# Performance work log

Hardware: AMD Instinct MI355X
Metric: run time of the kernel (lower is better)

The kernel has to match this reference:

```python
import jax, jax.numpy as jnp
import numpy as np

B, N, D = 2, 512, 64
EPS = 1e-5  # BatchNorm eps (torch default)


def setup_inputs() -> dict:
    key = jax.random.key(0)

    def k(i):
        return jax.random.fold_in(key, i)

    inp = {}
    inp["node_features"] = jax.random.normal(k(0), (B, N, D), jnp.float32)
    inp["node_masks"] = jax.random.randint(k(1), (B, N), 0, 2) > 0
    lin_dims = [(128, 2 * D), (64, 128), (32, 64), (1, 32)]
    for i, (o, ii) in enumerate(lin_dims, start=1):
        inp[f"W{i}"] = jax.random.normal(k(10 + i), (o, ii), jnp.float32) * np.float32(1.0 / np.sqrt(ii))
        inp[f"b{i}"] = jnp.zeros((o,), jnp.float32)
    for i, o in enumerate([128, 64, 32], start=1):
        inp[f"g{i}"] = jnp.ones((o,), jnp.float32) + 0.1 * jax.random.normal(k(20 + i), (o,), jnp.float32)
        inp[f"be{i}"] = 0.1 * jax.random.normal(k(30 + i), (o,), jnp.float32)
        inp[f"m{i}"] = jnp.zeros((o,), jnp.float32)
        inp[f"v{i}"] = jnp.ones((o,), jnp.float32)
    return inp


def _bn(x, g, be, m, v):
    # eval-mode BatchNorm1d with running stats
    return (x - m) * (g * jax.lax.rsqrt(v + EPS)) + be


def _edge_predictor(node_features, node_masks,
                    W1, b1, g1, be1, m1, v1,
                    W2, b2, g2, be2, m2, v2,
                    W3, b3, g3, be3, m3, v3,
                    W4, b4):
    Bq, Nq, Dq = node_features.shape
    # pairwise features: concat(f_i, f_j) -> [B, N, N, 2D]
    fi = jnp.broadcast_to(node_features[:, :, None, :], (Bq, Nq, Nq, Dq))
    fj = jnp.broadcast_to(node_features[:, None, :, :], (Bq, Nq, Nq, Dq))
    pair = jnp.concatenate([fi, fj], axis=-1)
    # 3-layer MLP + BN (eval) + ReLU, then scalar head (dropout is identity in eval)
    x = jax.nn.relu(_bn(jnp.einsum('bijk,ok->bijo', pair, W1) + b1, g1, be1, m1, v1))
    x = jax.nn.relu(_bn(jnp.einsum('bijk,ok->bijo', x, W2) + b2, g2, be2, m2, v2))
    x = jax.nn.relu(_bn(jnp.einsum('bijk,ok->bijo', x, W3) + b3, g3, be3, m3, v3))
    logits = (jnp.einsum('bijk,ok->bijo', x, W4) + b4)[..., 0]  # [B, N, N]
    # diagonal -> -10, symmetrize
    eye = jnp.eye(Nq, dtype=bool)
    logits = jnp.where(eye[None], jnp.float32(-10.0), logits)
    logits = (logits + jnp.swapaxes(logits, 1, 2)) * 0.5
    # cosine-similarity boost (F.normalize eps = 1e-12)
    norm = jnp.maximum(jnp.linalg.norm(node_features, axis=-1, keepdims=True), 1e-12)
    nf = node_features / norm
    sim = jnp.einsum('bnd,bmd->bnm', nf, nf)
    logits = (logits + 2.0 * sim) / 0.5  # temperature 0.5
    probs = jax.nn.sigmoid(logits)
    probs = jnp.where(probs > 0.6, probs * 1.2, probs * 0.8)
    probs = jnp.clip(probs, 0.0, 1.0)
    # scatter into dense adjacency only at valid (i, j) pairs; batches with
    # n_valid <= 1 are skipped (stay zero) as in the torch loop
    n_valid = jnp.sum(node_masks, axis=-1)  # [B]
    active = (n_valid > 1)[:, None, None]
    pair_mask = node_masks[:, :, None] & node_masks[:, None, :] & active
    adjacency = jnp.where(pair_mask, probs, 0.0)
    adjacency_logits = jnp.where(pair_mask, logits, 0.0)
    return adjacency, adjacency_logits


def reference(node_features, node_masks,
              W1, b1, g1, be1, m1, v1,
              W2, b2, g2, be2, m2, v2,
              W3, b3, g3, be3, m3, v3,
              W4, b4):
    return _edge_predictor(node_features, node_masks,
                           W1, b1, g1, be1, m1, v1,
                           W2, b2, g2, be2, m2, v2,
                           W3, b3, g3, be3, m3, v3,
                           W4, b4)
```

## Files before the change

kernel.cpp:

```cpp
#include <hip/hip_runtime.h>
#include <math.h>

#define BB 2
#define NN2 512
#define DD 64
#define EPS 1e-5f

#define OFF_W1TA  0
#define OFF_W1TB  8192
#define OFF_VBIAS 16384
#define OFF_W2T   16512
#define OFF_C2    24704
#define OFF_W3T   24768
#define OFF_C3    26816
#define OFF_U     26848
#define OFF_V     157920
#define OFF_NF    288992
#define OFF_RAWL  354528
#define OFF_NVALID 878816

__global__ __launch_bounds__(256) void prep_fold(
    const float* __restrict__ W1, const float* __restrict__ b1,
    const float* __restrict__ W2, const float* __restrict__ b2,
    const float* __restrict__ W3, const float* __restrict__ b3,
    const float* __restrict__ g1, const float* __restrict__ be1,
    const float* __restrict__ m1, const float* __restrict__ v1,
    const float* __restrict__ g2, const float* __restrict__ be2,
    const float* __restrict__ m2, const float* __restrict__ v2,
    const float* __restrict__ g3, const float* __restrict__ be3,
    const float* __restrict__ m3, const float* __restrict__ v3,
    const int* __restrict__ masks,
    float* __restrict__ ws, int* __restrict__ nvalid)
{
    const int blk = blockIdx.x, t = threadIdx.x;
    if (blk < 8) {
        int e0 = blk * 1024 + t * 4;
        #pragma unroll
        for (int q = 0; q < 4; q++) {
            int e = e0 + q;
            int o = e & 63, k = e >> 6;
            float s = g2[o] * rsqrtf(v2[o] + EPS);
            ws[OFF_W2T + e] = W2[o * 128 + k] * s;
        }
    } else if (blk < 10) {
        int e0 = (blk - 8) * 1024 + t * 4;
        #pragma unroll
        for (int q = 0; q < 4; q++) {
            int e = e0 + q;
            if (e < 2048) {
                int o = e & 31, k = e >> 5;
                float s = g3[o] * rsqrtf(v3[o] + EPS);
                ws[OFF_W3T + e] = W3[o * 64 + k] * s;
            }
        }
    } else if (blk < 26) {
        int e0 = (blk - 10) * 1024 + t * 4;
        #pragma unroll
        for (int q = 0; q < 4; q++) {
            int e = e0 + q;
            if (e < 8192) {
                int d = e >> 7, o = e & 127;
                float s = g1[o] * rsqrtf(v1[o] + EPS);
                ws[OFF_W1TA + e] = W1[o * 128 + d] * s;
            } else {
                int eb = e - 8192;
                int d = eb >> 7, o = eb & 127;
                float s = g1[o] * rsqrtf(v1[o] + EPS);
                ws[OFF_W1TB + eb] = W1[o * 128 + 64 + d] * s;
            }
        }
    } else if (blk == 26) {
        if (t < 128) {
            float s = g1[t] * rsqrtf(v1[t] + EPS);
            ws[OFF_VBIAS + t] = s * b1[t] + be1[t] - m1[t] * s;
        } else if (t < 192) {
            int o = t - 128;
            float s = g2[o] * rsqrtf(v2[o] + EPS);
            ws[OFF_C2 + o] = b2[o] * s + be2[o] - m2[o] * s;
        } else if (t < 224) {
            int o = t - 192;
            float s = g3[o] * rsqrtf(v3[o] + EPS);
            ws[OFF_C3 + o] = b3[o] * s + be3[o] - m3[o] * s;
        }
    } else {
        int w = t >> 6, l = t & 63;
        if (w < BB) {
            int s = 0;
            #pragma unroll
            for (int q = 0; q < 8; q++) s += (masks[w * NN2 + q * 64 + l] != 0) ? 1 : 0;
            #pragma unroll
            for (int off = 1; off < 64; off <<= 1) s += __shfl_xor(s, off);
            if (l == 0) nvalid[w] = s;
        }
    }
}

__global__ __launch_bounds__(128) void prep_uv(
    const float* __restrict__ feat,
    const float* __restrict__ W1ta, const float* __restrict__ W1tb,
    const float* __restrict__ Vbias,
    float* __restrict__ U, float* __restrict__ V)
{
    __shared__ float F[4][64];
    const int nb = blockIdx.x * 4;
    const int t = threadIdx.x;
    if (t < 64) {
        int r = t >> 4, c = (t & 15) * 4;
        *(float4*)&F[r][c] = *(const float4*)&feat[(nb + r) * 64 + c];
    }
    __syncthreads();
    const int o = t;
    float aU[4] = {0.f, 0.f, 0.f, 0.f};
    float aV[4] = {0.f, 0.f, 0.f, 0.f};
    for (int d = 0; d < 64; d++) {
        float wa = W1ta[d * 128 + o];
        float wb = W1tb[d * 128 + o];
        #pragma unroll
        for (int n = 0; n < 4; n++) {
            aU[n] = fmaf(F[n][d], wa, aU[n]);
            aV[n] = fmaf(F[n][d], wb, aV[n]);
        }
    }
    float vb = Vbias[o];
    #pragma unroll
    for (int n = 0; n < 4; n++) {
        U[(nb + n) * 128 + o] = aU[n];
        V[(nb + n) * 128 + o] = aV[n] + vb;
    }
}

__global__ __launch_bounds__(256) void prep_nf(
    const float* __restrict__ feat, float* __restrict__ nf)
{
    const int t = threadIdx.x;
    const int w = t >> 6, l = t & 63;
    const int node = blockIdx.x * 4 + w;
    float x = feat[node * 64 + l];
    float ss = x * x;
    #pragma unroll
    for (int off = 1; off < 64; off <<= 1) ss += __shfl_xor(ss, off);
    float inv = 1.0f / fmaxf(sqrtf(ss), 1e-12f);
    nf[node * 64 + l] = x * inv;
}

__global__ __launch_bounds__(256) void mlp_main(
    const float* __restrict__ U, const float* __restrict__ V,
    const float* __restrict__ W2t, const float* __restrict__ c2,
    const float* __restrict__ W3t, const float* __restrict__ c3,
    const float* __restrict__ W4, const float* __restrict__ b4,
    float* __restrict__ rawL)
{
    __shared__ float Ut[16][132];
    __shared__ float Vt[16][132];
    const int t = threadIdx.x;
    const int b = blockIdx.z;
    const int i0 = blockIdx.y * 16, j0 = blockIdx.x * 16;
    {
        int r = t >> 4, c = (t & 15) * 8;
        float4 a0 = *(const float4*)&U[(b * NN2 + i0 + r) * 128 + c];
        float4 a1 = *(const float4*)&U[(b * NN2 + i0 + r) * 128 + c + 4];
        *(float4*)&Ut[r][c]     = a0;
        *(float4*)&Ut[r][c + 4] = a1;
        float4 v0 = *(const float4*)&V[(b * NN2 + j0 + r) * 128 + c];
        float4 v1 = *(const float4*)&V[(b * NN2 + j0 + r) * 128 + c + 4];
        *(float4*)&Vt[r][c]     = v0;
        *(float4*)&Vt[r][c + 4] = v1;
    }
    __syncthreads();
    const int i = t >> 4, j = t & 15;

    float acc[64];
    #pragma unroll
    for (int o = 0; o < 64; o++) acc[o] = c2[o];
    for (int k = 0; k < 128; k += 4) {
        float4 uk = *(const float4*)&Ut[i][k];
        float4 vk = *(const float4*)&Vt[j][k];
        float h[4];
        h[0] = fmaxf(uk.x + vk.x, 0.f);
        h[1] = fmaxf(uk.y + vk.y, 0.f);
        h[2] = fmaxf(uk.z + vk.z, 0.f);
        h[3] = fmaxf(uk.w + vk.w, 0.f);
        const float* w = &W2t[k * 64];
        #pragma unroll
        for (int kk = 0; kk < 4; kk++) {
            #pragma unroll
            for (int o = 0; o < 64; o++)
                acc[o] = fmaf(w[kk * 64 + o], h[kk], acc[o]);
        }
    }
    float a3[32];
    #pragma unroll
    for (int o = 0; o < 32; o++) a3[o] = c3[o];
    #pragma unroll
    for (int k = 0; k < 64; k++) {
        float hk = fmaxf(acc[k], 0.f);
        #pragma unroll
        for (int o = 0; o < 32; o++)
            a3[o] = fmaf(W3t[k * 32 + o], hk, a3[o]);
    }
    float lg = b4[0];
    #pragma unroll
    for (int k = 0; k < 32; k++) lg = fmaf(W4[k], fmaxf(a3[k], 0.f), lg);

    rawL[(size_t)(b * NN2 + i0 + i) * NN2 + j0 + j] = lg;
}

__global__ __launch_bounds__(256) void post_kernel(
    const float* __restrict__ rawL, const float* __restrict__ nf,
    const int* __restrict__ masks, const int* __restrict__ nvalid,
    float* __restrict__ outA, float* __restrict__ outL)
{
    __shared__ float nfI[16][68], nfJ[16][68];
    __shared__ float Lt[16][17];
    __shared__ int mI[16], mJ[16];
    const int t = threadIdx.x;
    const int b = blockIdx.z, i0 = blockIdx.y * 16, j0 = blockIdx.x * 16;
    {
        int r = t >> 4, c = (t & 15) * 4;
        *(float4*)&nfI[r][c] = *(const float4*)&nf[(b * NN2 + i0 + r) * 64 + c];
        *(float4*)&nfJ[r][c] = *(const float4*)&nf[(b * NN2 + j0 + r) * 64 + c];
    }
    {
        int r = t >> 4, c = t & 15;
        Lt[r][c] = rawL[(size_t)(b * NN2 + j0 + r) * NN2 + i0 + c];
    }
    if (t < 16) mI[t] = masks[b * NN2 + i0 + t];
    else if (t < 32) mJ[t - 16] = masks[b * NN2 + j0 + (t - 16)];
    __syncthreads();

    const int i = t >> 4, j = t & 15;
    const int gi = i0 + i, gj = j0 + j;
    float Lij = rawL[(size_t)(b * NN2 + gi) * NN2 + gj];
    float Lji = Lt[j][i];
    float Ls = (gi == gj) ? -10.0f : 0.5f * (Lij + Lji);

    float sim = 0.f;
    #pragma unroll
    for (int d = 0; d < 64; d += 4) {
        float4 x = *(const float4*)&nfI[i][d];
        float4 y = *(const float4*)&nfJ[j][d];
        sim = fmaf(x.x, y.x, sim);
        sim = fmaf(x.y, y.y, sim);
        sim = fmaf(x.z, y.z, sim);
        sim = fmaf(x.w, y.w, sim);
    }
    float logit = (Ls + 2.0f * sim) * 2.0f;
    float p = 1.0f / (1.0f + expf(-logit));
    p = (p > 0.6f) ? p * 1.2f : p * 0.8f;
    p = fminf(fmaxf(p, 0.0f), 1.0f);
    bool pm = (mI[i] != 0) && (mJ[j] != 0) && (nvalid[b] > 1);
    size_t idx = (size_t)(b * NN2 + gi) * NN2 + gj;
    outA[idx] = pm ? p : 0.0f;
    outL[idx] = pm ? logit : 0.0f;
}

extern "C" void kernel_launch(void* const* d_in, const int* in_sizes, int n_in,
                              void* d_out, int out_size, void* d_ws, size_t ws_size,
                              hipStream_t stream)
{
    const float* feat = (const float*)d_in[0];
    const int*   masks = (const int*)d_in[1];
    const float* W1 = (const float*)d_in[2];
    const float* b1 = (const float*)d_in[3];
    const float* W2 = (const float*)d_in[4];
    const float* b2 = (const float*)d_in[5];
    const float* W3 = (const float*)d_in[6];
    const float* b3 = (const float*)d_in[7];
    const float* W4 = (const float*)d_in[8];
    const float* b4 = (const float*)d_in[9];
    const float* g1 = (const float*)d_in[10];
    const float* be1 = (const float*)d_in[11];
    const float* m1 = (const float*)d_in[12];
    const float* v1 = (const float*)d_in[13];
    const float* g2 = (const float*)d_in[14];
    const float* be2 = (const float*)d_in[15];
    const float* m2 = (const float*)d_in[16];
    const float* v2 = (const float*)d_in[17];
    const float* g3 = (const float*)d_in[18];
    const float* be3 = (const float*)d_in[19];
    const float* m3 = (const float*)d_in[20];
    const float* v3 = (const float*)d_in[21];

    float* ws = (float*)d_ws;
    float* W1ta  = ws + OFF_W1TA;
    float* W1tb  = ws + OFF_W1TB;
    float* Vbias = ws + OFF_VBIAS;
    float* W2t   = ws + OFF_W2T;
    float* c2    = ws + OFF_C2;
    float* W3t   = ws + OFF_W3T;
    float* c3    = ws + OFF_C3;
    float* U     = ws + OFF_U;
    float* V     = ws + OFF_V;
    float* nf    = ws + OFF_NF;
    float* rawL  = ws + OFF_RAWL;
    int*   nvalid = (int*)(ws + OFF_NVALID);

    float* outA = (float*)d_out;
    float* outL = outA + (size_t)BB * NN2 * NN2;

    prep_fold<<<28, 256, 0, stream>>>(W1, b1, W2, b2, W3, b3,
                                      g1, be1, m1, v1, g2, be2, m2, v2,
                                      g3, be3, m3, v3, masks, ws, nvalid);
    prep_uv<<<256, 128, 0, stream>>>(feat, W1ta, W1tb, Vbias, U, V);
    prep_nf<<<256, 256, 0, stream>>>(feat, nf);
    dim3 grid(32, 32, 2);
    mlp_main<<<grid, 256, 0, stream>>>(U, V, W2t, c2, W3t, c3, W4, b4, rawL);
    post_kernel<<<grid, 256, 0, stream>>>(rawL, nf, masks, nvalid, outA, outL);
}
```

Measured before the change: 267.2 us.

## Fuse MLP and post-processing over symmetric tile pairs, merge nf into prep_uv

Launches one block per upper-triangular tile pair (i,j). Each block evaluates the MLP for both (i,j) and (j,i), exchanges the results through shared memory to symmetrize, and writes both output tiles directly. This removes the rawL round-trip through global memory and the separate post kernel. The per-node normalization is also moved into prep_uv, which drops one more launch. The MLP work is unchanged, but diagonal blocks do half the work of off-diagonal ones, which causes load imbalance, and the larger shared footprint together with the launch_bounds min-blocks hint may change occupancy.

```diff
diff --git a/kernel.cpp b/kernel.cpp
--- a/kernel.cpp
+++ b/kernel.cpp
@@ -3,8 +3,9 @@
 
 #define BB 2
 #define NN2 512
-#define DD 64
 #define EPS 1e-5f
+#define NT 32
+#define TP 528
 
 #define OFF_W1TA  0
 #define OFF_W1TB  8192
@@ -16,8 +17,7 @@
 #define OFF_U     26848
 #define OFF_V     157920
 #define OFF_NF    288992
-#define OFF_RAWL  354528
-#define OFF_NVALID 878816
+#define OFF_NVALID 354528
 
 __global__ __launch_bounds__(256) void prep_fold(
     const float* __restrict__ W1, const float* __restrict__ b1,
@@ -99,7 +99,7 @@
     const float* __restrict__ feat,
     const float* __restrict__ W1ta, const float* __restrict__ W1tb,
     const float* __restrict__ Vbias,
-    float* __restrict__ U, float* __restrict__ V)
+    float* __restrict__ U, float* __restrict__ V, float* __restrict__ nf)
 {
     __shared__ float F[4][64];
     const int nb = blockIdx.x * 4;
@@ -109,6 +109,21 @@
         *(float4*)&F[r][c] = *(const float4*)&feat[(nb + r) * 64 + c];
     }
     __syncthreads();
+    if (t < 64) {
+        int g = t >> 4, c0 = t & 15;
+        float x0 = F[g][c0],      x1 = F[g][c0 + 16];
+        float x2 = F[g][c0 + 32], x3 = F[g][c0 + 48];
+        float ss = x0 * x0 + x1 * x1 + x2 * x2 + x3 * x3;
+        ss += __shfl_xor(ss, 1);
+        ss += __shfl_xor(ss, 2);
+        ss += __shfl_xor(ss, 4);
+        ss += __shfl_xor(ss, 8);
+        float inv = 1.0f / fmaxf(sqrtf(ss), 1e-12f);
+        nf[(nb + g) * 64 + c0]      = x0 * inv;
+        nf[(nb + g) * 64 + c0 + 16] = x1 * inv;
+        nf[(nb + g) * 64 + c0 + 32] = x2 * inv;
+        nf[(nb + g) * 64 + c0 + 48] = x3 * inv;
+    }
     const int o = t;
     float aU[4] = {0.f, 0.f, 0.f, 0.f};
     float aV[4] = {0.f, 0.f, 0.f, 0.f};
@@ -129,129 +144,149 @@
     }
 }
 
-__global__ __launch_bounds__(256) void prep_nf(
-    const float* __restrict__ feat, float* __restrict__ nf)
-{
-    const int t = threadIdx.x;
-    const int w = t >> 6, l = t & 63;
-    const int node = blockIdx.x * 4 + w;
-    float x = feat[node * 64 + l];
-    float ss = x * x;
-    #pragma unroll
-    for (int off = 1; off < 64; off <<= 1) ss += __shfl_xor(ss, off);
-    float inv = 1.0f / fmaxf(sqrtf(ss), 1e-12f);
-    nf[node * 64 + l] = x * inv;
-}
-
-__global__ __launch_bounds__(256) void mlp_main(
+__device__ __forceinline__ float mlp_eval(
+    const float* Ur, const float* Vr,
+    const float* __restrict__ W2t, const float* __restrict__ c2,
+    const float* __restrict__ W3t, const float* __restrict__ c3,
+    const float* __restrict__ W4, float b40)
+{
+    float acc[64];
+    #pragma unroll
+    for (int o = 0; o < 64; o++) acc[o] = c2[o];
+    for (int k = 0; k < 128; k += 4) {
+        float4 uk = *(const float4*)&Ur[k];
+        float4 vk = *(const float4*)&Vr[k];
+        float h0 = fmaxf(uk.x + vk.x, 0.f);
+        float h1 = fmaxf(uk.y + vk.y, 0.f);
+        float h2 = fmaxf(uk.z + vk.z, 0.f);
+        float h3 = fmaxf(uk.w + vk.w, 0.f);
+        const float* w = &W2t[k * 64];
+        #pragma unroll
+        for (int o = 0; o < 64; o++) acc[o] = fmaf(w[o], h0, acc[o]);
+        #pragma unroll
+        for (int o = 0; o < 64; o++) acc[o] = fmaf(w[64 + o], h1, acc[o]);
+        #pragma unroll
+        for (int o = 0; o < 64; o++) acc[o] = fmaf(w[128 + o], h2, acc[o]);
+        #pragma unroll
+        for (int o = 0; o < 64; o++) acc[o] = fmaf(w[192 + o], h3, acc[o]);
+    }
+    float a3[32];
+    #pragma unroll
+    for (int o = 0; o < 32; o++) a3[o] = c3[o];
+    #pragma unroll
+    for (int k = 0; k < 64; k++) {
+        float hk = fmaxf(acc[k], 0.f);
+        #pragma unroll
+        for (int o = 0; o < 32; o++) a3[o] = fmaf(W3t[k * 32 + o], hk, a3[o]);
+    }
+    float lg = b40;
+    #pragma unroll
+    for (int k = 0; k < 32; k++) lg = fmaf(W4[k], fmaxf(a3[k], 0.f), lg);
+    return lg;
+}
+
+__global__ __launch_bounds__(256, 2) void mlp_fused(
     const float* __restrict__ U, const float* __restrict__ V,
+    const float* __restrict__ nf,
     const float* __restrict__ W2t, const float* __restrict__ c2,
     const float* __restrict__ W3t, const float* __restrict__ c3,
     const float* __restrict__ W4, const float* __restrict__ b4,
-    float* __restrict__ rawL)
-{
-    __shared__ float Ut[16][132];
-    __shared__ float Vt[16][132];
+    const int* __restrict__ masks, const int* __restrict__ nvalid,
+    float* __restrict__ outA, float* __restrict__ outL)
+{
+    __shared__ float Ui[16][132], Vj[16][132], Uj[16][132], Vi[16][132];
+    __shared__ float nfI[16][68], nfJ[16][68];
+    __shared__ float exA[16][17], exB[16][17];
+    __shared__ int mI[16], mJ[16];
+
     const int t = threadIdx.x;
     const int b = blockIdx.z;
-    const int i0 = blockIdx.y * 16, j0 = blockIdx.x * 16;
+    int tp = blockIdx.x, ti = 0;
+    while (tp >= NT - ti) { tp -= NT - ti; ti++; }
+    const int tj = ti + tp;
+    const int i0 = ti * 16, j0 = tj * 16;
+    const bool offd = (ti != tj);
+
     {
         int r = t >> 4, c = (t & 15) * 8;
-        float4 a0 = *(const float4*)&U[(b * NN2 + i0 + r) * 128 + c];
-        float4 a1 = *(const float4*)&U[(b * NN2 + i0 + r) * 128 + c + 4];
-        *(float4*)&Ut[r][c]     = a0;
-        *(float4*)&Ut[r][c + 4] = a1;
-        float4 v0 = *(const float4*)&V[(b * NN2 + j0 + r) * 128 + c];
-        float4 v1 = *(const float4*)&V[(b * NN2 + j0 + r) * 128 + c + 4];
-        *(float4*)&Vt[r][c]     = v0;
-        *(float4*)&Vt[r][c + 4] = v1;
-    }
-    __syncthreads();
-    const int i = t >> 4, j = t & 15;
-
-    float acc[64];
-    #pragma unroll
-    for (int o = 0; o < 64; o++) acc[o] = c2[o];
-    for (int k = 0; k < 128; k += 4) {
-        float4 uk = *(const float4*)&Ut[i][k];
-        float4 vk = *(const float4*)&Vt[j][k];
-        float h[4];
-        h[0] = fmaxf(uk.x + vk.x, 0.f);
-        h[1] = fmaxf(uk.y + vk.y, 0.f);
-        h[2] = fmaxf(uk.z + vk.z, 0.f);
-        h[3] = fmaxf(uk.w + vk.w, 0.f);
-        const float* w = &W2t[k * 64];
-        #pragma unroll
-        for (int kk = 0; kk < 4; kk++) {
-            #pragma unroll
-            for (int o = 0; o < 64; o++)
-                acc[o] = fmaf(w[kk * 64 + o], h[kk], acc[o]);
-        }
-    }
-    float a3[32];
-    #pragma unroll
-    for (int o = 0; o < 32; o++) a3[o] = c3[o];
-    #pragma unroll
-    for (int k = 0; k < 64; k++) {
-        float hk = fmaxf(acc[k], 0.f);
-        #pragma unroll
-        for (int o = 0; o < 32; o++)
-            a3[o] = fmaf(W3t[k * 32 + o], hk, a3[o]);
-    }
-    float lg = b4[0];
-    #pragma unroll
-    for (int k = 0; k < 32; k++) lg = fmaf(W4[k], fmaxf(a3[k], 0.f), lg);
-
-    rawL[(size_t)(b * NN2 + i0 + i) * NN2 + j0 + j] = lg;
-}
-
-__global__ __launch_bounds__(256) void post_kernel(
-    const float* __restrict__ rawL, const float* __restrict__ nf,
-    const int* __restrict__ masks, const int* __restrict__ nvalid,
-    float* __restrict__ outA, float* __restrict__ outL)
-{
-    __shared__ float nfI[16][68], nfJ[16][68];
-    __shared__ float Lt[16][17];
-    __shared__ int mI[16], mJ[16];
-    const int t = threadIdx.x;
-    const int b = blockIdx.z, i0 = blockIdx.y * 16, j0 = blockIdx.x * 16;
-    {
-        int r = t >> 4, c = (t & 15) * 4;
-        *(float4*)&nfI[r][c] = *(const float4*)&nf[(b * NN2 + i0 + r) * 64 + c];
-        *(float4*)&nfJ[r][c] = *(const float4*)&nf[(b * NN2 + j0 + r) * 64 + c];
-    }
-    {
-        int r = t >> 4, c = t & 15;
-        Lt[r][c] = rawL[(size_t)(b * NN2 + j0 + r) * NN2 + i0 + c];
+        const float* uI = &U[(size_t)(b * NN2 + i0 + r) * 128 + c];
+        const float* vJ = &V[(size_t)(b * NN2 + j0 + r) * 128 + c];
+        const float* uJ = &U[(size_t)(b * NN2 + j0 + r) * 128 + c];
+        const float* vI = &V[(size_t)(b * NN2 + i0 + r) * 128 + c];
+        *(float4*)&Ui[r][c]     = *(const float4*)uI;
+        *(float4*)&Ui[r][c + 4] = *(const float4*)(uI + 4);
+        *(float4*)&Vj[r][c]     = *(const float4*)vJ;
+        *(float4*)&Vj[r][c + 4] = *(const float4*)(vJ + 4);
+        *(float4*)&Uj[r][c]     = *(const float4*)uJ;
+        *(float4*)&Uj[r][c + 4] = *(const float4*)(uJ + 4);
+        *(float4*)&Vi[r][c]     = *(const float4*)vI;
+        *(float4*)&Vi[r][c + 4] = *(const float4*)(vI + 4);
+        int c4 = (t & 15) * 4;
+        *(float4*)&nfI[r][c4] = *(const float4*)&nf[(size_t)(b * NN2 + i0 + r) * 64 + c4];
+        *(float4*)&nfJ[r][c4] = *(const float4*)&nf[(size_t)(b * NN2 + j0 + r) * 64 + c4];
     }
     if (t < 16) mI[t] = masks[b * NN2 + i0 + t];
     else if (t < 32) mJ[t - 16] = masks[b * NN2 + j0 + (t - 16)];
     __syncthreads();
 
     const int i = t >> 4, j = t & 15;
-    const int gi = i0 + i, gj = j0 + j;
-    float Lij = rawL[(size_t)(b * NN2 + gi) * NN2 + gj];
-    float Lji = Lt[j][i];
-    float Ls = (gi == gj) ? -10.0f : 0.5f * (Lij + Lji);
-
-    float sim = 0.f;
-    #pragma unroll
-    for (int d = 0; d < 64; d += 4) {
-        float4 x = *(const float4*)&nfI[i][d];
-        float4 y = *(const float4*)&nfJ[j][d];
-        sim = fmaf(x.x, y.x, sim);
-        sim = fmaf(x.y, y.y, sim);
-        sim = fmaf(x.z, y.z, sim);
-        sim = fmaf(x.w, y.w, sim);
-    }
-    float logit = (Ls + 2.0f * sim) * 2.0f;
-    float p = 1.0f / (1.0f + expf(-logit));
-    p = (p > 0.6f) ? p * 1.2f : p * 0.8f;
-    p = fminf(fmaxf(p, 0.0f), 1.0f);
-    bool pm = (mI[i] != 0) && (mJ[j] != 0) && (nvalid[b] > 1);
-    size_t idx = (size_t)(b * NN2 + gi) * NN2 + gj;
-    outA[idx] = pm ? p : 0.0f;
-    outL[idx] = pm ? logit : 0.0f;
+    const float b40 = b4[0];
+
+    float LA = mlp_eval(&Ui[i][0], &Vj[j][0], W2t, c2, W3t, c3, W4, b40);
+    exA[i][j] = LA;
+    float LB = 0.f;
+    if (offd) {
+        LB = mlp_eval(&Uj[i][0], &Vi[j][0], W2t, c2, W3t, c3, W4, b40);
+        exB[i][j] = LB;
+    }
+    __syncthreads();
+    const float At = exA[j][i];
+    const float Bt = offd ? exB[j][i] : At;
+    const int nv = nvalid[b];
+
+    {
+        float sim = 0.f;
+        #pragma unroll
+        for (int d = 0; d < 64; d += 4) {
+            float4 x = *(const float4*)&nfI[i][d];
+            float4 y = *(const float4*)&nfJ[j][d];
+            sim = fmaf(x.x, y.x, sim);
+            sim = fmaf(x.y, y.y, sim);
+            sim = fmaf(x.z, y.z, sim);
+            sim = fmaf(x.w, y.w, sim);
+        }
+        const int gi = i0 + i, gj = j0 + j;
+        float Ls = (gi == gj) ? -10.0f : 0.5f * (LA + Bt);
+        float logit = (Ls + 2.0f * sim) * 2.0f;
+        float p = 1.0f / (1.0f + expf(-logit));
+        p = (p > 0.6f) ? p * 1.2f : p * 0.8f;
+        p = fminf(fmaxf(p, 0.0f), 1.0f);
+        bool pm = (mI[i] != 0) && (mJ[j] != 0) && (nv > 1);
+        size_t idx = (size_t)(b * NN2 + gi) * NN2 + gj;
+        outA[idx] = pm ? p : 0.0f;
+        outL[idx] = pm ? logit : 0.0f;
+    }
+    if (offd) {
+        float sim = 0.f;
+        #pragma unroll
+        for (int d = 0; d < 64; d += 4) {
+            float4 x = *(const float4*)&nfJ[i][d];
+            float4 y = *(const float4*)&nfI[j][d];
+            sim = fmaf(x.x, y.x, sim);
+            sim = fmaf(x.y, y.y, sim);
+            sim = fmaf(x.z, y.z, sim);
+            sim = fmaf(x.w, y.w, sim);
+        }
+        float Ls = 0.5f * (LB + At);
+        float logit = (Ls + 2.0f * sim) * 2.0f;
+        float p = 1.0f / (1.0f + expf(-logit));
+        p = (p > 0.6f) ? p * 1.2f : p * 0.8f;
+        p = fminf(fmaxf(p, 0.0f), 1.0f);
+        bool pm = (mJ[i] != 0) && (mI[j] != 0) && (nv > 1);
+        size_t idx = (size_t)(b * NN2 + j0 + i) * NN2 + (i0 + j);
+        outA[idx] = pm ? p : 0.0f;
+        outL[idx] = pm ? logit : 0.0f;
+    }
 }
 
 extern "C" void kernel_launch(void* const* d_in, const int* in_sizes, int n_in,
@@ -291,8 +326,7 @@
     float* c3    = ws + OFF_C3;
     float* U     = ws + OFF_U;
     float* V     = ws + OFF_V;
-    float* nf    = ws + OFF_NF;
-    float* rawL  = ws + OFF_RAWL;
+    float* nfp   = ws + OFF_NF;
     int*   nvalid = (int*)(ws + OFF_NVALID);
 
     float* outA = (float*)d_out;
@@ -301,9 +335,8 @@
     prep_fold<<<28, 256, 0, stream>>>(W1, b1, W2, b2, W3, b3,
                                       g1, be1, m1, v1, g2, be2, m2, v2,
                                       g3, be3, m3, v3, masks, ws, nvalid);
-    prep_uv<<<256, 128, 0, stream>>>(feat, W1ta, W1tb, Vbias, U, V);
-    prep_nf<<<256, 256, 0, stream>>>(feat, nf);
-    dim3 grid(32, 32, 2);
-    mlp_main<<<grid, 256, 0, stream>>>(U, V, W2t, c2, W3t, c3, W4, b4, rawL);
-    post_kernel<<<grid, 256, 0, stream>>>(rawL, nf, masks, nvalid, outA, outL);
-}
+    prep_uv<<<256, 128, 0, stream>>>(feat, W1ta, W1tb, Vbias, U, V, nfp);
+    dim3 grid(TP, 1, BB);
+    mlp_fused<<<grid, 256, 0, stream>>>(U, V, nfp, W2t, c2, W3t, c3, W4, b4,
+                                        masks, nvalid, outA, outL);
+}
```

Result: slower. 310.6 us (+16.3%).
